# Performance work log

Hardware: AMD Instinct MI355X
Metric: run time of the kernel (lower is better)

Reference implementation:

```python
import jax, jax.numpy as jnp
import numpy as np

NUM_HEADS = 32
NUM_KV_HEADS = 8
HEAD_DIM = 128
HIDDEN = 4096
ROPE_THETA = 10000.0
RMS_EPS = 1e-6


def setup_inputs() -> dict:
    key = jax.random.key(0)
    k1, k2, k3 = jax.random.split(key, 3)
    T = 2048
    qkv_out = (NUM_HEADS + 2 * NUM_KV_HEADS) * HEAD_DIM  # 6144
    return {
        "positions": jnp.arange(T, dtype=jnp.int64),
        "hidden_states": jax.random.normal(k1, (T, HIDDEN), dtype=jnp.float32),
        "wqkv": jax.random.normal(k2, (qkv_out, HIDDEN), dtype=jnp.float32) * 0.02,
        "wo": jax.random.normal(k3, (HIDDEN, NUM_HEADS * HEAD_DIM), dtype=jnp.float32) * 0.02,
        "q_norm_w": jnp.ones((HEAD_DIM,), dtype=jnp.float32),
        "k_norm_w": jnp.ones((HEAD_DIM,), dtype=jnp.float32),
    }


def _rms_norm(x, w):
    # per-head RMSNorm over last dim, computed in fp32 (matches Dots1RMSNorm)
    xf = x.astype(jnp.float32)
    var = jnp.mean(xf * xf, axis=-1, keepdims=True)
    return (w * (xf * jax.lax.rsqrt(var + RMS_EPS))).astype(x.dtype)


def _rope(x, positions):
    # NeoX-style rotary: rotate halves. x: [T, H, D]
    half = HEAD_DIM // 2
    inv_freq = 1.0 / (ROPE_THETA ** (jnp.arange(0, half, dtype=jnp.float32) / half))
    ang = positions.astype(jnp.float32)[:, None] * inv_freq  # [T, half]
    cos = jnp.cos(ang)[:, None, :]  # [T,1,half]
    sin = jnp.sin(ang)[:, None, :]
    x1, x2 = x[..., :half], x[..., half:]
    return jnp.concatenate([x1 * cos - x2 * sin, x2 * cos + x1 * sin], axis=-1)


def reference(positions, hidden_states, wqkv, wo, q_norm_w, k_norm_w):
    T = hidden_states.shape[0]
    q_size = NUM_HEADS * HEAD_DIM
    kv_size = NUM_KV_HEADS * HEAD_DIM
    qkv = hidden_states @ wqkv.T  # [T, q_size + 2*kv_size]
    q = qkv[:, :q_size].reshape(T, NUM_HEADS, HEAD_DIM)
    k = qkv[:, q_size:q_size + kv_size].reshape(T, NUM_KV_HEADS, HEAD_DIM)
    v = qkv[:, q_size + kv_size:].reshape(T, NUM_KV_HEADS, HEAD_DIM)

    q = _rms_norm(q, q_norm_w)
    k = _rms_norm(k, k_norm_w)
    q = _rope(q, positions)
    k = _rope(k, positions)

    # GQA: expand kv heads to query heads (group of 4)
    group = NUM_HEADS // NUM_KV_HEADS
    k = jnp.repeat(k, group, axis=1)  # [T, H, D]
    v = jnp.repeat(v, group, axis=1)

    scale = HEAD_DIM ** -0.5
    scores = jnp.einsum('thd,shd->hts', q, k) * scale  # [H, T, T]
    causal = positions[:, None] >= positions[None, :]
    scores = jnp.where(causal[None, :, :], scores, jnp.finfo(scores.dtype).min)
    probs = jax.nn.softmax(scores, axis=-1)
    attn = jnp.einsum('hts,shd->thd', probs, v)  # [T, H, D]
    out = attn.reshape(T, NUM_HEADS * HEAD_DIM) @ wo.T  # [T, HIDDEN]
    return out
```

## Files before the change

### kernel.cpp

```cpp
#include <hip/hip_runtime.h>


#define T_SEQ 2048
#define HID   4096
#define NH    32
#define NKVH  8
#define HD    128
#define QKVN  6144
#define QSZ   4096
#define QKN   5120

typedef unsigned short u16;
typedef __attribute__((ext_vector_type(8))) short short8;
typedef __attribute__((ext_vector_type(4))) float floatx4;

__device__ __forceinline__ float bf2f(u16 u) {
  union { unsigned int i; float f; } c; c.i = ((unsigned int)u) << 16; return c.f;
}
__device__ __forceinline__ u16 f2bf(float f) {
  union { float f; unsigned int i; } c; c.f = f;
  unsigned int u = c.i;
  return (u16)((u + 0x7FFFu + ((u >> 16) & 1u)) >> 16);
}
__device__ __forceinline__ floatx4 mfma16(short8 a, short8 b, floatx4 c) {
  return __builtin_amdgcn_mfma_f32_16x16x32_bf16(a, b, c, 0, 0, 0);
}

#define GLD16(g, l) __builtin_amdgcn_global_load_lds( \
    (__attribute__((address_space(1))) unsigned int*)(g), \
    (__attribute__((address_space(3))) unsigned int*)(l), 16, 0, 0)

__global__ __launch_bounds__(256) void cvt3_kernel(
    const float* __restrict__ s0, const float* __restrict__ s1,
    const float* __restrict__ s2, u16* __restrict__ d0, u16* __restrict__ d1,
    u16* __restrict__ d2, int n0, int n1, int n2) {
  int total = n0 + n1 + n2;
  int stride = gridDim.x * 256;
  for (int i = blockIdx.x * 256 + threadIdx.x; i < total; i += stride) {
    const float* s; u16* d; int j = i;
    if (j < n0)           { s = s0; d = d0; }
    else if (j < n0 + n1) { j -= n0; s = s1; d = d1; }
    else                  { j -= n0 + n1; s = s2; d = d2; }
    float4 v = ((const float4*)s)[j];
    ushort4 o;
    o.x = f2bf(v.x); o.y = f2bf(v.y); o.z = f2bf(v.z); o.w = f2bf(v.w);
    ((ushort4*)d)[j] = o;
  }
}

template <int MODE>
__global__ __launch_bounds__(256, 2) void gemm_bt(const u16* __restrict__ A,
    const u16* __restrict__ B, void* __restrict__ Cv, u16* __restrict__ VT,
    int mtiles, int K, int ldC) {
  __shared__ __attribute__((aligned(16))) u16 As[128 * 64];
  __shared__ __attribute__((aligned(16))) u16 Bs[128 * 64];
  const int tid = threadIdx.x;
  const int wave = tid >> 6, lane = tid & 63;
  const int lq = lane >> 4, lc = lane & 15;
  const int wm = wave >> 1, wn = wave & 1;
  const int by = blockIdx.x % mtiles, bx = blockIdx.x / mtiles;
  const int m0 = by * 128, n0 = bx * 128;

  floatx4 acc[4][4];
#pragma unroll
  for (int i = 0; i < 4; ++i)
#pragma unroll
    for (int j = 0; j < 4; ++j) acc[i][j] = {0.f, 0.f, 0.f, 0.f};

  int arow[4], brow[4];
#pragma unroll
  for (int i = 0; i < 4; ++i) {
    arow[i] = wm * 64 + i * 16 + lc;
    brow[i] = wn * 64 + i * 16 + lc;
  }

  const u16* asrc[4]; const u16* bsrc[4];
#pragma unroll
  for (int r = 0; r < 4; ++r) {
    int L = r * 256 + tid;
    int mm = L >> 3;
    int cc = (L & 7) ^ (mm & 7);
    asrc[r] = A + (size_t)(m0 + mm) * K + cc * 8;
    bsrc[r] = B + (size_t)(n0 + mm) * K + cc * 8;
  }

  for (int k0 = 0; k0 < K; k0 += 64) {
#pragma unroll
    for (int r = 0; r < 4; ++r) {
      GLD16(asrc[r] + k0, As + (r * 256 + wave * 64) * 8);
      GLD16(bsrc[r] + k0, Bs + (r * 256 + wave * 64) * 8);
    }
    __syncthreads();
#pragma unroll
    for (int kb = 0; kb < 2; ++kb) {
      short8 af[4], bfr[4];
#pragma unroll
      for (int mi = 0; mi < 4; ++mi)
        af[mi] = *(const short8*)&As[arow[mi] * 64 + (((kb * 4 + lq) ^ (arow[mi] & 7)) * 8)];
#pragma unroll
      for (int ni = 0; ni < 4; ++ni)
        bfr[ni] = *(const short8*)&Bs[brow[ni] * 64 + (((kb * 4 + lq) ^ (brow[ni] & 7)) * 8)];
#pragma unroll
      for (int mi = 0; mi < 4; ++mi)
#pragma unroll
        for (int ni = 0; ni < 4; ++ni)
          acc[mi][ni] = mfma16(af[mi], bfr[ni], acc[mi][ni]);
    }
    __syncthreads();
  }

  if (MODE == 1 && n0 >= 5120) {
#pragma unroll
    for (int mi = 0; mi < 4; ++mi) {
      int row = m0 + wm * 64 + mi * 16 + lq * 4;
#pragma unroll
      for (int ni = 0; ni < 4; ++ni) {
        int rel = n0 + wn * 64 + ni * 16 + lc - 5120;
        ushort4 u;
        u.x = f2bf(acc[mi][ni][0]); u.y = f2bf(acc[mi][ni][1]);
        u.z = f2bf(acc[mi][ni][2]); u.w = f2bf(acc[mi][ni][3]);
        *(ushort4*)&VT[(size_t)rel * T_SEQ + row] = u;
      }
    }
  } else {
#pragma unroll
    for (int mi = 0; mi < 4; ++mi) {
      int row = m0 + wm * 64 + mi * 16 + lq * 4;
#pragma unroll
      for (int ni = 0; ni < 4; ++ni) {
        int col = n0 + wn * 64 + ni * 16 + lc;
#pragma unroll
        for (int r = 0; r < 4; ++r) {
          if (MODE == 1)
            ((u16*)Cv)[(size_t)(row + r) * ldC + col] = f2bf(acc[mi][ni][r]);
          else
            ((float*)Cv)[(size_t)(row + r) * ldC + col] = acc[mi][ni][r];
        }
      }
    }
  }
}

__global__ __launch_bounds__(256) void norm_rope_kernel(const u16* __restrict__ qk,
    const float* __restrict__ qw, const float* __restrict__ kw,
    u16* __restrict__ Qo, u16* __restrict__ Ko) {
  const int t = blockIdx.x;
  const int hs = blockIdx.y * 4 + (threadIdx.x >> 6);
  const int l = threadIdx.x & 63;
  const bool isq = hs < NH;
  const int col0 = isq ? hs * HD : QSZ + (hs - NH) * HD;
  const u16* src = qk + (size_t)t * QKN + col0;
  float x1 = bf2f(src[l]);
  float x2 = bf2f(src[l + 64]);
  float ss = x1 * x1 + x2 * x2;
#pragma unroll
  for (int m = 1; m < 64; m <<= 1) ss += __shfl_xor(ss, m);
  float rstd = rsqrtf(ss * (1.0f / HD) + 1e-6f);
  const float* w = isq ? qw : kw;
  float n1 = x1 * rstd * w[l];
  float n2 = x2 * rstd * w[l + 64];
  float inv = exp2f((float)l * -0.20762050593045158f);
  float ang = (float)t * inv;
  float s, c;
  __sincosf(ang, &s, &c);
  float o1 = n1 * c - n2 * s;
  float o2 = n2 * c + n1 * s;
  if (isq) {
    o1 *= 0.08838834764831845f; o2 *= 0.08838834764831845f;
    u16* dst = Qo + ((size_t)hs * T_SEQ + t) * HD;
    dst[l] = f2bf(o1); dst[l + 64] = f2bf(o2);
  } else {
    u16* dst = Ko + ((size_t)(hs - NH) * T_SEQ + t) * HD;
    dst[l] = f2bf(o1); dst[l + 64] = f2bf(o2);
  }
}

__global__ __launch_bounds__(256, 2) void attn_kernel(const u16* __restrict__ Qg,
    const u16* __restrict__ Kg, const u16* __restrict__ VTg, u16* __restrict__ Og) {
  __shared__ __attribute__((aligned(16))) u16 Ks[8192];
  __shared__ __attribute__((aligned(16))) u16 Vs[2][8192];
  __shared__ __attribute__((aligned(16))) u16 Ps[8192];

  const int bid = blockIdx.x;
  const int h = bid & 31;
  const int qq = bid >> 5;
  const int qt = (qq < 8) ? (15 - qq) : (qq - 8);
  const int kvh = h >> 2;
  const int tid = threadIdx.x;
  const int wave = tid >> 6, lane = tid & 63;
  const int lq = lane >> 4, lc = lane & 15;

  const u16* kbase[4];
  const u16* vbase[4];
#pragma unroll
  for (int i = 0; i < 4; ++i) {
    int L = i * 256 + tid;
    int s = L >> 4, cp = L & 15;
    kbase[i] = Kg + ((size_t)kvh * T_SEQ + s) * HD + ((cp ^ (s & 15)) * 8);
    int d = L >> 3, cv = L & 7;
    vbase[i] = VTg + ((size_t)kvh * HD + d) * T_SEQ + ((cv ^ (d & 7)) * 8);
  }

  short8 qf[2][4];
#pragma unroll
  for (int mb = 0; mb < 2; ++mb)
#pragma unroll
    for (int ks = 0; ks < 4; ++ks) {
      int t = qt * 128 + wave * 32 + mb * 16 + lc;
      qf[mb][ks] = *(const short8*)&Qg[((size_t)h * T_SEQ + t) * HD + ks * 32 + lq * 8];
    }

  short8 ones;
#pragma unroll
  for (int j = 0; j < 8; ++j) ones[j] = (short)0x3F80;

  floatx4 of[2][8];
  floatx4 lacc[2];
#pragma unroll
  for (int mb = 0; mb < 2; ++mb) {
    lacc[mb] = {0.f, 0.f, 0.f, 0.f};
#pragma unroll
    for (int db = 0; db < 8; ++db) of[mb][db] = {0.f, 0.f, 0.f, 0.f};
  }

  const int ktmax = 2 * qt + 1;
  const int t0g = qt * 128 + wave * 32;
  const int wave_tmax = t0g + 31;

#pragma unroll
  for (int i = 0; i < 4; ++i) {
    GLD16(kbase[i], Ks + (i * 256 + wave * 64) * 8);
    GLD16(vbase[i], Vs[0] + (i * 256 + wave * 64) * 8);
  }

  for (int kt = 0; kt <= ktmax; ++kt) {
    __syncthreads();
    if (kt + 1 <= ktmax) {
      u16* vd = Vs[(kt + 1) & 1] + (size_t)wave * 64 * 8;
#pragma unroll
      for (int i = 0; i < 4; ++i)
        GLD16(vbase[i] + (kt + 1) * 64, vd + i * 256 * 8);
    }
    const bool active = (kt * 64) <= wave_tmax;
    if (active) {
      floatx4 sf[2][4];
#pragma unroll
      for (int mb = 0; mb < 2; ++mb)
#pragma unroll
        for (int nb = 0; nb < 4; ++nb) sf[mb][nb] = {0.f, 0.f, 0.f, 0.f};
#pragma unroll
      for (int ks = 0; ks < 4; ++ks) {
        short8 kf[4];
#pragma unroll
        for (int nb = 0; nb < 4; ++nb)
          kf[nb] = *(const short8*)&Ks[(nb * 16 + lc) * 128 + ((4 * ks + lq) ^ lc) * 8];
#pragma unroll
        for (int mb = 0; mb < 2; ++mb)
#pragma unroll
          for (int nb = 0; nb < 4; ++nb)
            sf[mb][nb] = mfma16(kf[nb], qf[mb][ks], sf[mb][nb]);
      }
      const bool nm = (kt * 64 + 63) > t0g;
#pragma unroll
      for (int mb = 0; mb < 2; ++mb) {
        const int trow = wave * 32 + mb * 16 + lc;
        const int tg = qt * 128 + trow;
#pragma unroll
        for (int nb = 0; nb < 4; ++nb) {
          ushort4 u;
          float p0 = __expf(sf[mb][nb][0]);
          float p1 = __expf(sf[mb][nb][1]);
          float p2 = __expf(sf[mb][nb][2]);
          float p3 = __expf(sf[mb][nb][3]);
          if (nm) {
            int sg = kt * 64 + nb * 16 + lq * 4;
            p0 = (sg + 0 <= tg) ? p0 : 0.f;
            p1 = (sg + 1 <= tg) ? p1 : 0.f;
            p2 = (sg + 2 <= tg) ? p2 : 0.f;
            p3 = (sg + 3 <= tg) ? p3 : 0.f;
          }
          u.x = f2bf(p0); u.y = f2bf(p1); u.z = f2bf(p2); u.w = f2bf(p3);
          int c = 2 * nb + (lq >> 1);
          *(ushort4*)&Ps[trow * 64 + ((c ^ (trow & 7)) * 8) + (lq & 1) * 4] = u;
        }
      }
    }
    __syncthreads();
    if (kt + 1 <= ktmax) {
      u16* kd = Ks + (size_t)wave * 64 * 8;
#pragma unroll
      for (int i = 0; i < 4; ++i)
        GLD16(kbase[i] + (size_t)(kt + 1) * 8192, kd + i * 256 * 8);
    }
    if (active) {
      const u16* vb = Vs[kt & 1];
      short8 pf[2][2];
#pragma unroll
      for (int mb = 0; mb < 2; ++mb)
#pragma unroll
        for (int k2 = 0; k2 < 2; ++k2) {
          int trow = wave * 32 + mb * 16 + lc;
          pf[mb][k2] =
              *(const short8*)&Ps[trow * 64 + (((4 * k2 + lq) ^ (lc & 7)) * 8)];
        }
#pragma unroll
      for (int k2 = 0; k2 < 2; ++k2) {
#pragma unroll
        for (int db = 0; db < 8; ++db) {
          short8 vf =
              *(const short8*)&vb[(db * 16 + lc) * 64 + (((4 * k2 + lq) ^ (lc & 7)) * 8)];
          of[0][db] = mfma16(pf[0][k2], vf, of[0][db]);
          of[1][db] = mfma16(pf[1][k2], vf, of[1][db]);
        }
        lacc[0] = mfma16(pf[0][k2], ones, lacc[0]);
        lacc[1] = mfma16(pf[1][k2], ones, lacc[1]);
      }
    }
  }
#pragma unroll
  for (int mb = 0; mb < 2; ++mb)
#pragma unroll
    for (int r = 0; r < 4; ++r) {
      float inv = 1.f / lacc[mb][r];
      int tg = qt * 128 + wave * 32 + mb * 16 + lq * 4 + r;
#pragma unroll
      for (int db = 0; db < 8; ++db)
        Og[(size_t)tg * QSZ + h * HD + db * 16 + lc] = f2bf(of[mb][db][r] * inv);
    }
}

extern "C" void kernel_launch(void* const* d_in, const int* in_sizes, int n_in,
                              void* d_out, int out_size, void* d_ws, size_t ws_size,
                              hipStream_t stream) {
  (void)in_sizes; (void)n_in; (void)out_size; (void)ws_size;
  const float* hidden = (const float*)d_in[1];
  const float* wqkv   = (const float*)d_in[2];
  const float* wo     = (const float*)d_in[3];
  const float* qw     = (const float*)d_in[4];
  const float* kw     = (const float*)d_in[5];
  float* out = (float*)d_out;
  char* ws = (char*)d_ws;

  u16* h_bf    = (u16*)(ws + 0);
  u16* wq_bf   = (u16*)(ws + 16777216);
  u16* wo_bf   = (u16*)(ws + 67108864);
  u16* vT_bf   = (u16*)(ws + 100663296);
  u16* qk_bf   = (u16*)(ws + 104857600);
  u16* q_bf    = (u16*)(ws + 16777216);
  u16* k_bf    = (u16*)(ws + 33554432);
  u16* attn_bf = (u16*)(ws + 0);

  cvt3_kernel<<<8192, 256, 0, stream>>>(
      hidden, wqkv, wo, h_bf, wq_bf, wo_bf,
      T_SEQ * HID / 4, QKVN * HID / 4, HID * QSZ / 4);

  gemm_bt<1><<<768, 256, 0, stream>>>(h_bf, wq_bf, qk_bf, vT_bf,
                                      T_SEQ / 128, HID, QKN);

  norm_rope_kernel<<<dim3(T_SEQ, 10), 256, 0, stream>>>(
      qk_bf, qw, kw, q_bf, k_bf);

  attn_kernel<<<512, 256, 0, stream>>>(q_bf, k_bf, vT_bf, attn_bf);

  gemm_bt<0><<<512, 256, 0, stream>>>(attn_bf, wo_bf, out, vT_bf,
                                      T_SEQ / 128, HID, QSZ);
}
```

Baseline: 486.5 us.

## Keep softmax probabilities in registers via shuffles and double-buffer K tiles

The attention kernel no longer writes the probability tile to LDS and reads it back. It repacks the bf16 P fragments across lanes with __shfl into the MFMA A-operand layout, which removes one __syncthreads per key tile. K is now double-buffered like V, so the next K and V tiles are prefetched together at the top of each iteration. The GEMMs also switch from a 1D grid with modulo decode to a 2D grid with N on x, which changes block rasterization and cache reuse. The trade-off is 16 shuffles per k-step in place of LDS traffic, plus a different L2 reuse pattern in the GEMMs.

Result: slower. 516.8 us (+6.2%).

```diff
diff --git a/kernel.cpp b/kernel.cpp
--- a/kernel.cpp
+++ b/kernel.cpp
@@ -11,16 +11,20 @@
 #define QKN   5120
 
 typedef unsigned short u16;
+typedef unsigned int u32;
 typedef __attribute__((ext_vector_type(8))) short short8;
 typedef __attribute__((ext_vector_type(4))) float floatx4;
 
 __device__ __forceinline__ float bf2f(u16 u) {
-  union { unsigned int i; float f; } c; c.i = ((unsigned int)u) << 16; return c.f;
+  union { u32 i; float f; } c; c.i = ((u32)u) << 16; return c.f;
 }
 __device__ __forceinline__ u16 f2bf(float f) {
-  union { float f; unsigned int i; } c; c.f = f;
-  unsigned int u = c.i;
+  union { float f; u32 i; } c; c.f = f;
+  u32 u = c.i;
   return (u16)((u + 0x7FFFu + ((u >> 16) & 1u)) >> 16);
+}
+__device__ __forceinline__ u32 pack2(float a, float b) {
+  return (u32)f2bf(a) | ((u32)f2bf(b) << 16);
 }
 __device__ __forceinline__ floatx4 mfma16(short8 a, short8 b, floatx4 c) {
   return __builtin_amdgcn_mfma_f32_16x16x32_bf16(a, b, c, 0, 0, 0);
@@ -51,15 +55,14 @@
 template <int MODE>
 __global__ __launch_bounds__(256, 2) void gemm_bt(const u16* __restrict__ A,
     const u16* __restrict__ B, void* __restrict__ Cv, u16* __restrict__ VT,
-    int mtiles, int K, int ldC) {
+    int K, int ldC) {
   __shared__ __attribute__((aligned(16))) u16 As[128 * 64];
   __shared__ __attribute__((aligned(16))) u16 Bs[128 * 64];
   const int tid = threadIdx.x;
   const int wave = tid >> 6, lane = tid & 63;
   const int lq = lane >> 4, lc = lane & 15;
   const int wm = wave >> 1, wn = wave & 1;
-  const int by = blockIdx.x % mtiles, bx = blockIdx.x / mtiles;
-  const int m0 = by * 128, n0 = bx * 128;
+  const int m0 = blockIdx.y * 128, n0 = blockIdx.x * 128;
 
   floatx4 acc[4][4];
 #pragma unroll
@@ -177,9 +180,8 @@
 
 __global__ __launch_bounds__(256, 2) void attn_kernel(const u16* __restrict__ Qg,
     const u16* __restrict__ Kg, const u16* __restrict__ VTg, u16* __restrict__ Og) {
-  __shared__ __attribute__((aligned(16))) u16 Ks[8192];
+  __shared__ __attribute__((aligned(16))) u16 Ks[2][8192];
   __shared__ __attribute__((aligned(16))) u16 Vs[2][8192];
-  __shared__ __attribute__((aligned(16))) u16 Ps[8192];
 
   const int bid = blockIdx.x;
   const int h = bid & 31;
@@ -226,23 +228,31 @@
   const int ktmax = 2 * qt + 1;
   const int t0g = qt * 128 + wave * 32;
   const int wave_tmax = t0g + 31;
+  const int s0l = ((lq & 1) * 2) * 16 + lc;
+  const int s1l = s0l + 16;
+  const int hi = lq >> 1;
 
 #pragma unroll
   for (int i = 0; i < 4; ++i) {
-    GLD16(kbase[i], Ks + (i * 256 + wave * 64) * 8);
+    GLD16(kbase[i], Ks[0] + (i * 256 + wave * 64) * 8);
     GLD16(vbase[i], Vs[0] + (i * 256 + wave * 64) * 8);
   }
 
   for (int kt = 0; kt <= ktmax; ++kt) {
     __syncthreads();
-    if (kt + 1 <= ktmax) {
-      u16* vd = Vs[(kt + 1) & 1] + (size_t)wave * 64 * 8;
-#pragma unroll
-      for (int i = 0; i < 4; ++i)
-        GLD16(vbase[i] + (kt + 1) * 64, vd + i * 256 * 8);
+    if (kt < ktmax) {
+      u16* kd = Ks[(kt + 1) & 1] + wave * 512;
+      u16* vd = Vs[(kt + 1) & 1] + wave * 512;
+#pragma unroll
+      for (int i = 0; i < 4; ++i) {
+        GLD16(kbase[i] + (size_t)(kt + 1) * 8192, kd + i * 2048);
+        GLD16(vbase[i] + (kt + 1) * 64, vd + i * 2048);
+      }
     }
     const bool active = (kt * 64) <= wave_tmax;
     if (active) {
+      const u16* kbuf = Ks[kt & 1];
+      const u16* vbuf = Vs[kt & 1];
       floatx4 sf[2][4];
 #pragma unroll
       for (int mb = 0; mb < 2; ++mb)
@@ -253,7 +263,7 @@
         short8 kf[4];
 #pragma unroll
         for (int nb = 0; nb < 4; ++nb)
-          kf[nb] = *(const short8*)&Ks[(nb * 16 + lc) * 128 + ((4 * ks + lq) ^ lc) * 8];
+          kf[nb] = *(const short8*)&kbuf[(nb * 16 + lc) * 128 + ((4 * ks + lq) ^ lc) * 8];
 #pragma unroll
         for (int mb = 0; mb < 2; ++mb)
 #pragma unroll
@@ -261,13 +271,12 @@
             sf[mb][nb] = mfma16(kf[nb], qf[mb][ks], sf[mb][nb]);
       }
       const bool nm = (kt * 64 + 63) > t0g;
+      u32 Dm[2][4][2];
 #pragma unroll
       for (int mb = 0; mb < 2; ++mb) {
-        const int trow = wave * 32 + mb * 16 + lc;
-        const int tg = qt * 128 + trow;
+        const int tg = qt * 128 + wave * 32 + mb * 16 + lc;
 #pragma unroll
         for (int nb = 0; nb < 4; ++nb) {
-          ushort4 u;
           float p0 = __expf(sf[mb][nb][0]);
           float p1 = __expf(sf[mb][nb][1]);
           float p2 = __expf(sf[mb][nb][2]);
@@ -279,41 +288,39 @@
             p2 = (sg + 2 <= tg) ? p2 : 0.f;
             p3 = (sg + 3 <= tg) ? p3 : 0.f;
           }
-          u.x = f2bf(p0); u.y = f2bf(p1); u.z = f2bf(p2); u.w = f2bf(p3);
-          int c = 2 * nb + (lq >> 1);
-          *(ushort4*)&Ps[trow * 64 + ((c ^ (trow & 7)) * 8) + (lq & 1) * 4] = u;
+          Dm[mb][nb][0] = pack2(p0, p1);
+          Dm[mb][nb][1] = pack2(p2, p3);
         }
       }
-    }
-    __syncthreads();
-    if (kt + 1 <= ktmax) {
-      u16* kd = Ks + (size_t)wave * 64 * 8;
-#pragma unroll
-      for (int i = 0; i < 4; ++i)
-        GLD16(kbase[i] + (size_t)(kt + 1) * 8192, kd + i * 256 * 8);
-    }
-    if (active) {
-      const u16* vb = Vs[kt & 1];
-      short8 pf[2][2];
-#pragma unroll
-      for (int mb = 0; mb < 2; ++mb)
-#pragma unroll
-        for (int k2 = 0; k2 < 2; ++k2) {
-          int trow = wave * 32 + mb * 16 + lc;
-          pf[mb][k2] =
-              *(const short8*)&Ps[trow * 64 + (((4 * k2 + lq) ^ (lc & 7)) * 8)];
+#pragma unroll
+      for (int k2 = 0; k2 < 2; ++k2) {
+        short8 pf[2];
+#pragma unroll
+        for (int mb = 0; mb < 2; ++mb) {
+          u32 a0 = (u32)__shfl((int)Dm[mb][2 * k2][0], s0l);
+          u32 b0 = (u32)__shfl((int)Dm[mb][2 * k2 + 1][0], s0l);
+          u32 a1 = (u32)__shfl((int)Dm[mb][2 * k2][1], s0l);
+          u32 b1 = (u32)__shfl((int)Dm[mb][2 * k2 + 1][1], s0l);
+          u32 a2 = (u32)__shfl((int)Dm[mb][2 * k2][0], s1l);
+          u32 b2 = (u32)__shfl((int)Dm[mb][2 * k2 + 1][0], s1l);
+          u32 a3 = (u32)__shfl((int)Dm[mb][2 * k2][1], s1l);
+          u32 b3 = (u32)__shfl((int)Dm[mb][2 * k2 + 1][1], s1l);
+          union { u32 u[4]; short8 s8; } cv;
+          cv.u[0] = hi ? b0 : a0;
+          cv.u[1] = hi ? b1 : a1;
+          cv.u[2] = hi ? b2 : a2;
+          cv.u[3] = hi ? b3 : a3;
+          pf[mb] = cv.s8;
         }
-#pragma unroll
-      for (int k2 = 0; k2 < 2; ++k2) {
 #pragma unroll
         for (int db = 0; db < 8; ++db) {
           short8 vf =
-              *(const short8*)&vb[(db * 16 + lc) * 64 + (((4 * k2 + lq) ^ (lc & 7)) * 8)];
-          of[0][db] = mfma16(pf[0][k2], vf, of[0][db]);
-          of[1][db] = mfma16(pf[1][k2], vf, of[1][db]);
+              *(const short8*)&vbuf[(db * 16 + lc) * 64 + (((4 * k2 + lq) ^ (lc & 7)) * 8)];
+          of[0][db] = mfma16(pf[0], vf, of[0][db]);
+          of[1][db] = mfma16(pf[1], vf, of[1][db]);
         }
-        lacc[0] = mfma16(pf[0][k2], ones, lacc[0]);
-        lacc[1] = mfma16(pf[1][k2], ones, lacc[1]);
+        lacc[0] = mfma16(pf[0], ones, lacc[0]);
+        lacc[1] = mfma16(pf[1], ones, lacc[1]);
       }
     }
   }
@@ -354,14 +361,14 @@
       hidden, wqkv, wo, h_bf, wq_bf, wo_bf,
       T_SEQ * HID / 4, QKVN * HID / 4, HID * QSZ / 4);
 
-  gemm_bt<1><<<768, 256, 0, stream>>>(h_bf, wq_bf, qk_bf, vT_bf,
-                                      T_SEQ / 128, HID, QKN);
+  gemm_bt<1><<<dim3(QKVN / 128, T_SEQ / 128), 256, 0, stream>>>(
+      h_bf, wq_bf, qk_bf, vT_bf, HID, QKN);
 
   norm_rope_kernel<<<dim3(T_SEQ, 10), 256, 0, stream>>>(
       qk_bf, qw, kw, q_bf, k_bf);
 
   attn_kernel<<<512, 256, 0, stream>>>(q_bf, k_bf, vT_bf, attn_bf);
 
-  gemm_bt<0><<<512, 256, 0, stream>>>(attn_bf, wo_bf, out, vT_bf,
-                                      T_SEQ / 128, HID, QSZ);
-}
+  gemm_bt<0><<<dim3(QSZ / 128, T_SEQ / 128), 256, 0, stream>>>(
+      attn_bf, wo_bf, out, vT_bf, HID, QSZ);
+}
```
